# Performance work log

Hardware: AMD Instinct MI355X
Metric: run time of the kernel (lower is better)

Reference implementation:

```python
import jax, jax.numpy as jnp
import numpy as np

NUM_EMBEDDINGS = 1024
EMBEDDING_DIM = 256
COMMITMENT_COST = 0.25


def setup_inputs() -> dict:
    key = jax.random.key(0)
    k_z, k_e = jax.random.split(key)
    z = jax.random.normal(k_z, (4, EMBEDDING_DIM, 16, 32, 32), dtype=jnp.float32)
    # torch init: uniform_(-1/K, 1/K)
    emb = jax.random.uniform(
        k_e, (NUM_EMBEDDINGS, EMBEDDING_DIM), dtype=jnp.float32,
        minval=-1.0 / NUM_EMBEDDINGS, maxval=1.0 / NUM_EMBEDDINGS)
    return {"z": z, "emb": emb}


def reference(z, emb):
    sg = jax.lax.stop_gradient
    b, c, d, h, w = z.shape
    K = emb.shape[0]
    # (B,C,D,H,W) -> (N, C)
    z_flat = jnp.transpose(z, (0, 2, 3, 4, 1)).reshape(-1, c)
    x_sq = jnp.sum(z_flat * z_flat, axis=1, keepdims=True)          # (N,1)
    e_sq = jnp.sum(emb * emb, axis=1)                                # (K,)
    xe = z_flat @ emb.T                                              # (N,K)
    distances = x_sq + e_sq[None, :] - 2.0 * xe
    encoding_indices = jnp.argmin(distances, axis=1)                 # (N,)
    z_q = emb[encoding_indices].reshape(b, d, h, w, c).transpose(0, 4, 1, 2, 3)
    embedding_loss = jnp.mean((sg(z_q) - z) ** 2)
    commitment_loss = COMMITMENT_COST * jnp.mean((z_q - sg(z)) ** 2)
    vq_loss = embedding_loss + commitment_loss
    z_q_st = z + sg(z_q - z)  # straight-through
    # perplexity from codebook usage histogram (== mean of one-hot encodings)
    counts = jnp.zeros((K,), z_flat.dtype).at[encoding_indices].add(1.0)
    avg_probs = counts / z_flat.shape[0]
    perplexity = jnp.exp(-jnp.sum(avg_probs * jnp.log(avg_probs + 1e-10)))
    return z_q_st, vq_loss, perplexity, encoding_indices.reshape(b, d, h, w)
```

## Files before the change

### kernel.cpp

```cpp
#include <hip/hip_runtime.h>


#define C_DIM 256
#define K_CODES 1024
#define N_VEC 65536
#define T_GAP 6e-4f

#define OUT_ZQ_SIZE 16777216
#define OUT_LOSS_OFF 16777216
#define OUT_PP_OFF   16777217
#define OUT_IDX_OFF  16777218

#define WS_EH    0
#define WS_EL    524288
#define WS_ESQ   1048576
#define WS_XSQ   1052672
#define WS_CNT   1314816
#define WS_LOSS  1318912
#define WS_FLC   1318920
#define WS_FLIST 1581072
#define WS_PM1   1843264
#define WS_EMBT  1843264
#define WS_PM2   2891840
#define WS_PIX   3940416

typedef __attribute__((ext_vector_type(8))) short short8;
typedef __attribute__((ext_vector_type(8))) unsigned short ushort8;
typedef __attribute__((ext_vector_type(16))) float f32x16;

__device__ __forceinline__ unsigned short bf16_rne(float v) {
    unsigned u = __float_as_uint(v);
    unsigned r = (u + 0x7FFFu + ((u >> 16) & 1u)) >> 16;
    return (unsigned short)r;
}



__global__ __launch_bounds__(256) void convert_z_kernel(const float* __restrict__ z,
                                                        unsigned short* __restrict__ zhF,
                                                        float* __restrict__ xsq) {
#pragma clang fp contract(off)
    __shared__ float tile[128][65];
    const int tid = threadIdx.x;
    const int ln = tid & 63;
    const int og = tid >> 6;
    const int n0 = blockIdx.x * 64;
    const int b = n0 >> 14, s0 = n0 & 16383;
    const int n = n0 + ln;
    const size_t tbase = (size_t)(n >> 5) * 8192;
    const int lr = n & 31;
    float res = 0.0f;

    for (int p = 0; p < 2; ++p) {
        __syncthreads();
        for (int i = 0; i < 32; ++i) {
            int c = p * 128 + i * 4 + og;
            tile[i * 4 + og][ln] = z[((size_t)b << 22) + ((size_t)c << 14) + s0 + ln];
        }
        __syncthreads();
#pragma unroll
        for (int t = 0; t < 4; ++t) {
            int oh = og + t * 4;
            int o  = p * 16 + oh;
            ushort8 hb;
#pragma unroll
            for (int j = 0; j < 8; ++j)
                hb[j] = bf16_rne(tile[oh * 8 + j][ln]);
            size_t off = tbase + (size_t)(o >> 1) * 512 + (size_t)(lr + 32 * (o & 1)) * 8;
            *reinterpret_cast<ushort8*>(zhF + off) = hb;
        }
        if (tid < 64) {
            float r[8];
#pragma unroll
            for (int j = 0; j < 8; ++j) { float v = tile[j][tid]; r[j] = v * v; }
#pragma unroll
            for (int i = 8; i < 128; i += 8)
#pragma unroll
                for (int j = 0; j < 8; ++j) { float v = tile[i + j][tid]; float t2 = v * v; r[j] = r[j] + t2; }
            float blk = ((r[0] + r[1]) + (r[2] + r[3])) + ((r[4] + r[5]) + (r[6] + r[7]));
            res = (p == 0) ? blk : res + blk;
        }
    }
    if (tid < 64) xsq[n0 + tid] = res;
}

__device__ __forceinline__ float pairwise_sq_128(const float* p) {
#pragma clang fp contract(off)
    float r[8];
#pragma unroll
    for (int j = 0; j < 8; ++j) { float v = p[j]; r[j] = v * v; }
#pragma unroll
    for (int i = 8; i < 128; i += 8)
#pragma unroll
        for (int j = 0; j < 8; ++j) { float v = p[i + j]; float t = v * v; r[j] = r[j] + t; }
    return ((r[0] + r[1]) + (r[2] + r[3])) + ((r[4] + r[5]) + (r[6] + r[7]));
}

__global__ __launch_bounds__(256) void convert_e_kernel(const float* __restrict__ emb,
                                                        unsigned short* __restrict__ ehF,
                                                        unsigned short* __restrict__ elF,
                                                        float* __restrict__ esq) {
#pragma clang fp contract(off)
    int t = blockIdx.x * 256 + threadIdx.x;
    int k = t >> 5, o = t & 31;
    int c0 = o * 8;
    ushort8 hb, lb;
#pragma unroll
    for (int j = 0; j < 8; ++j) {
        float v = emb[k * C_DIM + c0 + j];
        unsigned short h = bf16_rne(v);
        hb[j] = h;
        lb[j] = bf16_rne(v - __uint_as_float((unsigned)h << 16));
    }
    size_t off = (size_t)(k >> 5) * 8192 + (size_t)(o >> 1) * 512 + (size_t)((k & 31) + 32 * (o & 1)) * 8;
    *reinterpret_cast<ushort8*>(ehF + off) = hb;
    *reinterpret_cast<ushort8*>(elF + off) = lb;
    if (threadIdx.x < 8) {
        int k8 = blockIdx.x * 8 + threadIdx.x;
        const float* row = emb + (size_t)k8 * C_DIM;
        esq[k8] = pairwise_sq_128(row) + pairwise_sq_128(row + 128);
    }
}

__global__ __launch_bounds__(256) void transpose_kernel(const float* __restrict__ emb,
                                                        float* __restrict__ embT) {
    __shared__ float t[64][65];
    const int k0 = blockIdx.x * 64;
    const int c0 = blockIdx.y * 64;
    const int tx = threadIdx.x & 63, ty = threadIdx.x >> 6;
    for (int r = ty; r < 64; r += 4)
        t[r][tx] = emb[(k0 + r) * C_DIM + c0 + tx];
    __syncthreads();
    for (int r = ty; r < 64; r += 4)
        embT[(c0 + r) * K_CODES + k0 + tx] = t[tx][r];
}


__global__ __launch_bounds__(512, 1) void screen_kernel(
    const unsigned short* __restrict__ zhF,
    const unsigned short* __restrict__ ehF, const unsigned short* __restrict__ elF,
    const float* __restrict__ esq, const float* __restrict__ xsq,
    float* __restrict__ pm1, float* __restrict__ pm2,
    unsigned short* __restrict__ pix) {
    __shared__ __align__(16) unsigned short abuf[3][32 * 512];
    __shared__ float xbuf[1024];
    __shared__ float smp1[2][8][64], smp2[2][8][64];
    __shared__ int   smi[2][8][64];

    const int tid = threadIdx.x;
    const int w = tid >> 6, l = tid & 63, lr = l & 31, lh = l >> 5;
    const int bid = blockIdx.x;
    const int v = (bid & 7) * 32 + (bid >> 3);
    const int nb = v >> 2, kb = v & 3;
    const int n0 = nb * 1024;
    const int kw = kb * 256 + w * 32;
    const int loff = l * 8;

    short8 Eh[16], El[16];
    {
        const unsigned short* bh = ehF + (size_t)(kb * 8 + w) * 8192 + loff;
        const unsigned short* bl = elF + (size_t)(kb * 8 + w) * 8192 + loff;
#pragma unroll
        for (int q = 0; q < 16; ++q) {
            Eh[q] = *reinterpret_cast<const short8*>(bh + q * 512);
            El[q] = *reinterpret_cast<const short8*>(bl + q * 512);
        }
    }
    float esql[16];
#pragma unroll
    for (int r = 0; r < 16; ++r)
        esql[r] = esq[kw + (r & 3) + 8 * (r >> 2) + 4 * lh];

    __builtin_amdgcn_global_load_lds(
        (const __attribute__((address_space(1))) void*)(xsq + n0 + w * 64 + l),
        (__attribute__((address_space(3))) void*)&xbuf[w * 64], 4, 0, 0);
    __builtin_amdgcn_global_load_lds(
        (const __attribute__((address_space(1))) void*)(xsq + n0 + 512 + w * 64 + l),
        (__attribute__((address_space(3))) void*)&xbuf[512 + w * 64], 4, 0, 0);

    asm volatile("s_waitcnt vmcnt(0)" ::: "memory");
    __builtin_amdgcn_s_barrier();

#define STAGE(S) do {                                                                   \
    const int _b = (S) % 3;                                                             \
    _Pragma("unroll")                                                                   \
    for (int ci = 0; ci < 4; ++ci) {                                                    \
        int c = 4 * w + ci;                                                             \
        const unsigned short* src = zhF                                                 \
            + (size_t)((n0 >> 5) + (S) * 2 + (c >> 4)) * 8192                           \
            + (size_t)(c & 15) * 512 + loff;                                            \
        __builtin_amdgcn_global_load_lds(                                               \
            (const __attribute__((address_space(1))) void*)src,                         \
            (__attribute__((address_space(3))) void*)&abuf[_b][c * 512], 16, 0, 0);     \
    }                                                                                   \
} while (0)

    STAGE(0);
    STAGE(1);

    float rmA1 = 3.4e38f, rmA2 = 3.4e38f, rmB1 = 3.4e38f, rmB2 = 3.4e38f;
    int   riA = 0, riB = 0;

    for (int s = 0; s < 16; ++s) {
        const int cur = s % 3;
        if (s == 15) { asm volatile("s_waitcnt vmcnt(0) lgkmcnt(0)" ::: "memory"); }
        else         { asm volatile("s_waitcnt vmcnt(4) lgkmcnt(0)" ::: "memory"); }
        __builtin_amdgcn_s_barrier();
        __builtin_amdgcn_sched_barrier(0);
        if (s < 14) STAGE(s + 2);
        __builtin_amdgcn_sched_barrier(0);

        if (s >= 1 && ((s - 1) & 7) == w) {
            const int pp = (s - 1) & 1;
            float m1 = smp1[pp][0][l], m2 = smp2[pp][0][l];
            int i1 = smi[pp][0][l];
#pragma unroll
            for (int ww = 1; ww < 8; ++ww) {
                float q1 = smp1[pp][ww][l], q2 = smp2[pp][ww][l];
                int qi = smi[pp][ww][l];
                if (q1 < m1)      { m2 = fminf(m1, q2); m1 = q1; i1 = qi; }
                else if (q1 > m1) { m2 = fminf(m2, q1); }
                else              { m2 = m1; }
            }
            if (s - 1 == w) { rmA1 = m1; rmA2 = m2; riA = i1; }
            else            { rmB1 = m1; rmB2 = m2; riB = i1; }
        }

        f32x16 aH0, aL0, aH1, aL1;
#pragma unroll
        for (int r = 0; r < 16; ++r) { aH0[r] = 0.0f; aL0[r] = 0.0f; aH1[r] = 0.0f; aL1[r] = 0.0f; }

        __builtin_amdgcn_s_setprio(1);
#pragma unroll
        for (int q = 0; q < 16; ++q) {
            short8 azh0 = *reinterpret_cast<const short8*>(&abuf[cur][(q)      * 512 + loff]);
            short8 azh1 = *reinterpret_cast<const short8*>(&abuf[cur][(16 + q) * 512 + loff]);
            aH0 = __builtin_amdgcn_mfma_f32_32x32x16_bf16(Eh[q], azh0, aH0, 0, 0, 0);
            aL0 = __builtin_amdgcn_mfma_f32_32x32x16_bf16(El[q], azh0, aL0, 0, 0, 0);
            aH1 = __builtin_amdgcn_mfma_f32_32x32x16_bf16(Eh[q], azh1, aH1, 0, 0, 0);
            aL1 = __builtin_amdgcn_mfma_f32_32x32x16_bf16(El[q], azh1, aL1, 0, 0, 0);
        }
        __builtin_amdgcn_s_setprio(0);

#pragma unroll
        for (int i = 0; i < 2; ++i) {
            const f32x16 aH = i ? aH1 : aH0;
            const f32x16 aL = i ? aL1 : aL0;
            const float xs = xbuf[s * 64 + i * 32 + lr];
            float m1 = 3.4e38f, m2 = 3.4e38f;
            int i1 = 0;
#pragma unroll
            for (int r = 0; r < 16; ++r) {
                float dot = aH[r] + aL[r];
                float sv = (xs + esql[r]) - 2.0f * dot;
                int kg = kw + (r & 3) + 8 * (r >> 2) + 4 * lh;
                if (sv < m1) { m2 = m1; m1 = sv; i1 = kg; }
                else m2 = fminf(m2, sv);
            }
            float om1 = __shfl_xor(m1, 32, 64);
            float om2 = __shfl_xor(m2, 32, 64);
            int   oi  = __shfl_xor(i1, 32, 64);
            if (om1 < m1)      { m2 = fminf(m1, om2); m1 = om1; i1 = oi; }
            else if (om1 > m1) { m2 = fminf(m2, om1); }
            else               { m2 = m1; i1 = min(i1, oi); }
            if (lh == 0) {
                smp1[s & 1][w][i * 32 + lr] = m1;
                smp2[s & 1][w][i * 32 + lr] = m2;
                smi [s & 1][w][i * 32 + lr] = i1;
            }
        }
    }
#undef STAGE

    asm volatile("s_waitcnt lgkmcnt(0)" ::: "memory");
    __builtin_amdgcn_s_barrier();
    if (w == 7) {
        float m1 = smp1[1][0][l], m2 = smp2[1][0][l];
        int i1 = smi[1][0][l];
#pragma unroll
        for (int ww = 1; ww < 8; ++ww) {
            float q1 = smp1[1][ww][l], q2 = smp2[1][ww][l];
            int qi = smi[1][ww][l];
            if (q1 < m1)      { m2 = fminf(m1, q2); m1 = q1; i1 = qi; }
            else if (q1 > m1) { m2 = fminf(m2, q1); }
            else              { m2 = m1; }
        }
        rmB1 = m1; rmB2 = m2; riB = i1;
    }

    {
        size_t pA = (size_t)kb * N_VEC + n0 + w * 64 + l;
        size_t pB = (size_t)kb * N_VEC + n0 + (w + 8) * 64 + l;
        pm1[pA] = rmA1; pm2[pA] = rmA2; pix[pA] = (unsigned short)riA;
        pm1[pB] = rmB1; pm2[pB] = rmB2; pix[pB] = (unsigned short)riB;
    }
}

__global__ __launch_bounds__(256) void merge_kernel(
    const float* __restrict__ pm1, const float* __restrict__ pm2,
    const unsigned short* __restrict__ pix,
    unsigned* __restrict__ flag_list, unsigned* __restrict__ flag_count,
    float* __restrict__ out_idx, unsigned* __restrict__ counts) {
    int n = blockIdx.x * 256 + threadIdx.x;
    float m1 = 3.4e38f, m2 = 3.4e38f;
    int i1 = 0;
    for (int kb = 0; kb < 4; ++kb) {
        size_t p = (size_t)kb * N_VEC + n;
        float a1 = pm1[p], a2 = pm2[p];
        int ai = (int)pix[p];
        if (a1 < m1)      { m2 = fminf(m1, a2); m1 = a1; i1 = ai; }
        else if (a1 > m1) { m2 = fminf(m2, a1); }
        else              { m2 = m1; i1 = min(i1, ai); }
    }
    if (m2 - m1 <= T_GAP) {
        unsigned pos = atomicAdd(flag_count, 1u);
        flag_list[pos] = (unsigned)n;
    } else {
        out_idx[n] = (float)i1;
        atomicAdd(&counts[i1], 1u);
    }
}


__global__ __launch_bounds__(256) void refine_kernel(
    const float* __restrict__ z, const float* __restrict__ embT,
    const float* __restrict__ esq, const float* __restrict__ xsq,
    const unsigned* __restrict__ flag_list, const unsigned* __restrict__ flag_count,
    float* __restrict__ out_idx, unsigned* __restrict__ counts) {
#pragma clang fp contract(off)
    __shared__ float zrow[8][256];
    __shared__ int nrow[8];
    __shared__ unsigned long long red[8][4];
    const int tid = threadIdx.x;
    const unsigned cnt = *flag_count;
    const unsigned groups = (cnt + 7) >> 3;
    const int kbase = tid * 4;
    for (unsigned g = blockIdx.x; g < groups; g += gridDim.x) {
        __syncthreads();
        if (tid < 8) nrow[tid] = (g * 8 + tid < cnt) ? (int)flag_list[g * 8 + tid] : -1;
        __syncthreads();
        for (int r = 0; r < 8; ++r) {
            int n = nrow[r];
            if (n >= 0) {
                int b = n >> 14, s = n & 16383;
                zrow[r][tid] = z[((size_t)b << 22) + ((size_t)tid << 14) + s];
            }
        }
        __syncthreads();
        float acc[8][4];
#pragma unroll
        for (int r = 0; r < 8; ++r)
#pragma unroll
            for (int j = 0; j < 4; ++j) acc[r][j] = 0.0f;
        for (int c4 = 0; c4 < 64; ++c4) {
            float4 ek[4];
#pragma unroll
            for (int x = 0; x < 4; ++x)
                ek[x] = *reinterpret_cast<const float4*>(embT + (size_t)(c4 * 4 + x) * K_CODES + kbase);
#pragma unroll
            for (int r = 0; r < 8; ++r) {
                float4 zv = *reinterpret_cast<const float4*>(&zrow[r][c4 * 4]);
                float a;
                a = acc[r][0];
                a = fmaf(zv.x, ek[0].x, a); a = fmaf(zv.y, ek[1].x, a);
                a = fmaf(zv.z, ek[2].x, a); a = fmaf(zv.w, ek[3].x, a);
                acc[r][0] = a;
                a = acc[r][1];
                a = fmaf(zv.x, ek[0].y, a); a = fmaf(zv.y, ek[1].y, a);
                a = fmaf(zv.z, ek[2].y, a); a = fmaf(zv.w, ek[3].y, a);
                acc[r][1] = a;
                a = acc[r][2];
                a = fmaf(zv.x, ek[0].z, a); a = fmaf(zv.y, ek[1].z, a);
                a = fmaf(zv.z, ek[2].z, a); a = fmaf(zv.w, ek[3].z, a);
                acc[r][2] = a;
                a = acc[r][3];
                a = fmaf(zv.x, ek[0].w, a); a = fmaf(zv.y, ek[1].w, a);
                a = fmaf(zv.z, ek[2].w, a); a = fmaf(zv.w, ek[3].w, a);
                acc[r][3] = a;
            }
        }
        float esql[4];
#pragma unroll
        for (int j = 0; j < 4; ++j) esql[j] = esq[kbase + j];
#pragma unroll
        for (int r = 0; r < 8; ++r) {
            int n = nrow[r];
            float xs = (n >= 0) ? xsq[n] : 0.0f;
            float m = 3.4e38f;
            int mi = 0;
#pragma unroll
            for (int j = 0; j < 4; ++j) {
                float t1 = xs + esql[j];
                float d = t1 - 2.0f * acc[r][j];
                if (d < m) { m = d; mi = kbase + j; }
            }
            unsigned long long p = ((unsigned long long)__float_as_uint(m) << 32) | (unsigned)mi;
            for (int off = 32; off >= 1; off >>= 1) {
                unsigned long long o = __shfl_xor(p, off, 64);
                p = (o < p) ? o : p;
            }
            if ((tid & 63) == 0) red[r][tid >> 6] = p;
        }
        __syncthreads();
        if (tid < 8 && nrow[tid] >= 0) {
            unsigned long long p = red[tid][0];
#pragma unroll
            for (int ww = 1; ww < 4; ++ww) { unsigned long long o = red[tid][ww]; p = (o < p) ? o : p; }
            int idx = (int)(p & 0xFFFFFFFFull);
            out_idx[nrow[tid]] = (float)idx;
            atomicAdd(&counts[idx], 1u);
        }
    }
}


__global__ __launch_bounds__(256) void gather_kernel(
    const float* __restrict__ z, const float* __restrict__ embT,
    const float* __restrict__ out_idx, float* __restrict__ out,
    double* __restrict__ loss_acc) {
    const int tid = threadIdx.x;
    const int ct = blockIdx.x & 3;
    const int st = (blockIdx.x >> 2) & 15;
    const int b  = blockIdx.x >> 6;
    const int s0 = st * 1024;
    const int c0 = ct * 64;

    int idx[4];
#pragma unroll
    for (int q = 0; q < 4; ++q)
        idx[q] = (int)out_idx[(b << 14) + s0 + 4 * tid + q];

    const float* zb = z + ((size_t)b << 22) + s0 + 4 * tid;
    float* ob = out + ((size_t)b << 22) + s0 + 4 * tid;

    double local = 0.0;
    for (int c = 0; c < 64; ++c) {
        const int cg = c0 + c;
        const float* er = embT + (size_t)cg * K_CODES;
        float4 zv = *reinterpret_cast<const float4*>(zb + ((size_t)cg << 14));
        float4 ov;
        float d0 = er[idx[0]] - zv.x;
        float d1 = er[idx[1]] - zv.y;
        float d2 = er[idx[2]] - zv.z;
        float d3 = er[idx[3]] - zv.w;
        ov.x = zv.x + d0; ov.y = zv.y + d1; ov.z = zv.z + d2; ov.w = zv.w + d3;
        *reinterpret_cast<float4*>(ob + ((size_t)cg << 14)) = ov;
        local += (double)d0 * d0 + (double)d1 * d1 + (double)d2 * d2 + (double)d3 * d3;
    }
    for (int off = 32; off >= 1; off >>= 1) local += __shfl_down(local, off, 64);
    __shared__ double redd[4];
    if ((tid & 63) == 0) redd[tid >> 6] = local;
    __syncthreads();
    if (tid == 0) atomicAdd(loss_acc, redd[0] + redd[1] + redd[2] + redd[3]);
}

__global__ void finalize_kernel(const unsigned* __restrict__ counts,
                                const double* __restrict__ loss_acc,
                                float* __restrict__ out) {
    int tid = threadIdx.x;
    double s = 0.0;
    for (int k = tid; k < K_CODES; k += 256) {
        float avg = (float)counts[k] / 65536.0f;
        float t = avg * logf(avg + 1e-10f);
        s += (double)t;
    }
    for (int off = 32; off >= 1; off >>= 1) s += __shfl_down(s, off, 64);
    __shared__ double red[4];
    if ((tid & 63) == 0) red[tid >> 6] = s;
    __syncthreads();
    if (tid == 0) {
        double tot = red[0] + red[1] + red[2] + red[3];
        out[OUT_PP_OFF]   = expf((float)(-tot));
        out[OUT_LOSS_OFF] = 1.25f * (float)(loss_acc[0] / 16777216.0);
    }
}

extern "C" void kernel_launch(void* const* d_in, const int* in_sizes, int n_in,
                              void* d_out, int out_size, void* d_ws, size_t ws_size,
                              hipStream_t stream) {
    const float* z   = (const float*)d_in[0];
    const float* emb = (const float*)d_in[1];
    float* out = (float*)d_out;
    char* ws = (char*)d_ws;

    unsigned short* ehF = (unsigned short*)(ws + WS_EH);
    unsigned short* elF = (unsigned short*)(ws + WS_EL);
    float*    esq       = (float*)(ws + WS_ESQ);
    float*    xsq       = (float*)(ws + WS_XSQ);
    unsigned* counts    = (unsigned*)(ws + WS_CNT);
    double*   loss_acc  = (double*)(ws + WS_LOSS);
    unsigned* flag_cnt  = (unsigned*)(ws + WS_FLC);
    unsigned* flist     = (unsigned*)(ws + WS_FLIST);
    float*    pm1       = (float*)(ws + WS_PM1);
    float*    pm2       = (float*)(ws + WS_PM2);
    unsigned short* pix = (unsigned short*)(ws + WS_PIX);
    float*    embT      = (float*)(ws + WS_EMBT);

    unsigned short* zhF = (unsigned short*)out;
    float* out_idx = out + OUT_IDX_OFF;

    hipMemsetAsync(ws + WS_CNT, 0, 4108, stream);

    convert_z_kernel<<<1024, 256, 0, stream>>>(z, zhF, xsq);
    convert_e_kernel<<<128, 256, 0, stream>>>(emb, ehF, elF, esq);
    screen_kernel<<<256, 512, 0, stream>>>(zhF, ehF, elF, esq, xsq, pm1, pm2, pix);
    merge_kernel<<<256, 256, 0, stream>>>(pm1, pm2, pix, flist, flag_cnt, out_idx, counts);
    transpose_kernel<<<dim3(16, 4), 256, 0, stream>>>(emb, embT);
    refine_kernel<<<1024, 256, 0, stream>>>(z, embT, esq, xsq, flist, flag_cnt, out_idx, counts);
    gather_kernel<<<256, 256, 0, stream>>>(z, embT, out_idx, out, loss_acc);
    finalize_kernel<<<1, 256, 0, stream>>>(counts, loss_acc, out);
}
```

Measured before the change: 245.3 us.

## Load screen-kernel activations directly from global into registers instead of LDS pipeline

Removes the triple-buffered global-to-LDS staging of the bf16 activation tiles and the LDS copy of xsq. Each wave now loads its A fragments straight from global memory into registers, prefetching one k-step ahead, and reads xsq from global. This cuts LDS traffic, LDS footprint and pipeline bookkeeping. In exchange the MFMA loop depends on global load latency with only one step of lookahead. All 8 waves also read the same activation tile redundantly, relying on cache hits.

```diff
diff --git a/kernel.cpp b/kernel.cpp
--- a/kernel.cpp
+++ b/kernel.cpp
@@ -142,8 +142,6 @@
     const float* __restrict__ esq, const float* __restrict__ xsq,
     float* __restrict__ pm1, float* __restrict__ pm2,
     unsigned short* __restrict__ pix) {
-    __shared__ __align__(16) unsigned short abuf[3][32 * 512];
-    __shared__ float xbuf[1024];
     __shared__ float smp1[2][8][64], smp2[2][8][64];
     __shared__ int   smi[2][8][64];
 
@@ -171,44 +169,12 @@
     for (int r = 0; r < 16; ++r)
         esql[r] = esq[kw + (r & 3) + 8 * (r >> 2) + 4 * lh];
 
-    __builtin_amdgcn_global_load_lds(
-        (const __attribute__((address_space(1))) void*)(xsq + n0 + w * 64 + l),
-        (__attribute__((address_space(3))) void*)&xbuf[w * 64], 4, 0, 0);
-    __builtin_amdgcn_global_load_lds(
-        (const __attribute__((address_space(1))) void*)(xsq + n0 + 512 + w * 64 + l),
-        (__attribute__((address_space(3))) void*)&xbuf[512 + w * 64], 4, 0, 0);
-
-    asm volatile("s_waitcnt vmcnt(0)" ::: "memory");
-    __builtin_amdgcn_s_barrier();
-
-#define STAGE(S) do {                                                                   \
-    const int _b = (S) % 3;                                                             \
-    _Pragma("unroll")                                                                   \
-    for (int ci = 0; ci < 4; ++ci) {                                                    \
-        int c = 4 * w + ci;                                                             \
-        const unsigned short* src = zhF                                                 \
-            + (size_t)((n0 >> 5) + (S) * 2 + (c >> 4)) * 8192                           \
-            + (size_t)(c & 15) * 512 + loff;                                            \
-        __builtin_amdgcn_global_load_lds(                                               \
-            (const __attribute__((address_space(1))) void*)src,                         \
-            (__attribute__((address_space(3))) void*)&abuf[_b][c * 512], 16, 0, 0);     \
-    }                                                                                   \
-} while (0)
-
-    STAGE(0);
-    STAGE(1);
-
     float rmA1 = 3.4e38f, rmA2 = 3.4e38f, rmB1 = 3.4e38f, rmB2 = 3.4e38f;
     int   riA = 0, riB = 0;
 
     for (int s = 0; s < 16; ++s) {
-        const int cur = s % 3;
-        if (s == 15) { asm volatile("s_waitcnt vmcnt(0) lgkmcnt(0)" ::: "memory"); }
-        else         { asm volatile("s_waitcnt vmcnt(4) lgkmcnt(0)" ::: "memory"); }
+        asm volatile("s_waitcnt lgkmcnt(0)" ::: "memory");
         __builtin_amdgcn_s_barrier();
-        __builtin_amdgcn_sched_barrier(0);
-        if (s < 14) STAGE(s + 2);
-        __builtin_amdgcn_sched_barrier(0);
 
         if (s >= 1 && ((s - 1) & 7) == w) {
             const int pp = (s - 1) & 1;
@@ -226,19 +192,29 @@
             else            { rmB1 = m1; rmB2 = m2; riB = i1; }
         }
 
+        const unsigned short* abase0 = zhF + (size_t)((n0 >> 5) + s * 2) * 8192 + loff;
+        const unsigned short* abase1 = abase0 + 8192;
+
         f32x16 aH0, aL0, aH1, aL1;
 #pragma unroll
         for (int r = 0; r < 16; ++r) { aH0[r] = 0.0f; aL0[r] = 0.0f; aH1[r] = 0.0f; aL1[r] = 0.0f; }
 
+        short8 a0 = *reinterpret_cast<const short8*>(abase0);
+        short8 a1 = *reinterpret_cast<const short8*>(abase1);
+
         __builtin_amdgcn_s_setprio(1);
 #pragma unroll
         for (int q = 0; q < 16; ++q) {
-            short8 azh0 = *reinterpret_cast<const short8*>(&abuf[cur][(q)      * 512 + loff]);
-            short8 azh1 = *reinterpret_cast<const short8*>(&abuf[cur][(16 + q) * 512 + loff]);
-            aH0 = __builtin_amdgcn_mfma_f32_32x32x16_bf16(Eh[q], azh0, aH0, 0, 0, 0);
-            aL0 = __builtin_amdgcn_mfma_f32_32x32x16_bf16(El[q], azh0, aL0, 0, 0, 0);
-            aH1 = __builtin_amdgcn_mfma_f32_32x32x16_bf16(Eh[q], azh1, aH1, 0, 0, 0);
-            aL1 = __builtin_amdgcn_mfma_f32_32x32x16_bf16(El[q], azh1, aL1, 0, 0, 0);
+            short8 b0, b1;
+            if (q < 15) {
+                b0 = *reinterpret_cast<const short8*>(abase0 + (q + 1) * 512);
+                b1 = *reinterpret_cast<const short8*>(abase1 + (q + 1) * 512);
+            }
+            aH0 = __builtin_amdgcn_mfma_f32_32x32x16_bf16(Eh[q], a0, aH0, 0, 0, 0);
+            aL0 = __builtin_amdgcn_mfma_f32_32x32x16_bf16(El[q], a0, aL0, 0, 0, 0);
+            aH1 = __builtin_amdgcn_mfma_f32_32x32x16_bf16(Eh[q], a1, aH1, 0, 0, 0);
+            aL1 = __builtin_amdgcn_mfma_f32_32x32x16_bf16(El[q], a1, aL1, 0, 0, 0);
+            if (q < 15) { a0 = b0; a1 = b1; }
         }
         __builtin_amdgcn_s_setprio(0);
 
@@ -246,7 +222,7 @@
         for (int i = 0; i < 2; ++i) {
             const f32x16 aH = i ? aH1 : aH0;
             const f32x16 aL = i ? aL1 : aL0;
-            const float xs = xbuf[s * 64 + i * 32 + lr];
+            const float xs = xsq[n0 + s * 64 + i * 32 + lr];
             float m1 = 3.4e38f, m2 = 3.4e38f;
             int i1 = 0;
 #pragma unroll
@@ -270,7 +246,6 @@
             }
         }
     }
-#undef STAGE
 
     asm volatile("s_waitcnt lgkmcnt(0)" ::: "memory");
     __builtin_amdgcn_s_barrier();
```

After: 336.6 us. 1.37x slower.
